# Performance work log

Measured on AMD Instinct MI355X. Metric: run time of the kernel, lower is better.

## Reference

```python
import jax, jax.numpy as jnp
import numpy as np

M, NC, NT, DX = 8, 1024, 512, 3
CHUNK = 512          # chunk_size
N_STEPS = 8          # n_steps (tol=0.0 -> torch early-stop never fires)
LR = 0.1
B1, B2, EPS = 0.9, 0.999, 1e-8
SQRT5 = 5.0 ** 0.5
LOG2PI = float(np.log(2.0 * np.pi))
NOISE_LB = 1e-4      # gpytorch GreaterThan(1e-4) noise constraint


def setup_inputs():
    key = jax.random.key(0)
    k1, k2, k3 = jax.random.split(key, 3)
    return {
        "xc": jax.random.normal(k1, (M, NC, DX), jnp.float32),
        "yc": jax.random.normal(k2, (M, NC, 1), jnp.float32),
        "xt": jax.random.normal(k3, (M, NT, DX), jnp.float32),
    }


def _kernel(x1, x2, ls, outscale):
    # ScaleKernel(MaternKernel(nu=2.5)); ls: [m,1,1], outscale: [m]
    xs1, xs2 = x1 / ls, x2 / ls
    d2 = (jnp.sum(xs1 * xs1, -1)[:, :, None]
          + jnp.sum(xs2 * xs2, -1)[:, None, :]
          - 2.0 * jnp.einsum('mnd,mkd->mnk', xs1, xs2))
    d2 = jnp.clip(d2, 1e-12, None)   # clamp like gpytorch dist for grad safety
    d = jnp.sqrt(d2)
    k = (1.0 + SQRT5 * d + (5.0 / 3.0) * d2) * jnp.exp(-SQRT5 * d)
    return outscale[:, None, None] * k


def _constrained(params):
    ls = jax.nn.softplus(params["raw_ls"])                          # [m,1,1]
    outscale = jax.nn.softplus(params["raw_os"])                    # [m]
    noise = jax.nn.softplus(params["raw_noise"][:, 0]) + NOISE_LB   # [m]
    return ls, outscale, noise


def _nll(params, x, y):
    # sum over tasks of -ExactMarginalLogLikelihood (gpytorch divides by n)
    ls, outscale, noise = _constrained(params)
    n = x.shape[1]
    K = _kernel(x, x, ls, outscale) + noise[:, None, None] * jnp.eye(n, dtype=x.dtype)
    L = jnp.linalg.cholesky(K)
    diff = y - params["const"][:, None]
    alpha = jax.scipy.linalg.cho_solve((L, True), diff[..., None])[..., 0]
    quad = jnp.sum(diff * alpha, -1)
    logdet = 2.0 * jnp.sum(jnp.log(jnp.diagonal(L, axis1=-2, axis2=-1)), -1)
    mll = -0.5 * (quad + logdet + n * LOG2PI) / n
    return jnp.sum(-mll)


def _adam_step(carry, x_sub, y_sub):
    p, m_, v_, t = carry
    g = jax.grad(_nll)(p, x_sub, y_sub)
    t = t + 1.0
    tm = jax.tree_util.tree_map
    m_ = tm(lambda a, gg: B1 * a + (1.0 - B1) * gg, m_, g)
    v_ = tm(lambda a, gg: B2 * a + (1.0 - B2) * gg * gg, v_, g)
    bc1 = 1.0 - B1 ** t
    bc2 = 1.0 - B2 ** t
    p = tm(lambda pp, mm, vv: pp - LR * (mm / bc1) / (jnp.sqrt(vv / bc2) + EPS), p, m_, v_)
    return (p, m_, v_, t)


def _gp_forward(xc, yc, xt):
    y = yc[..., 0]                                    # [m, nc]
    zl = lambda s: jnp.zeros(s, jnp.float32)
    # gpytorch raw params initialize to 0
    params = {"raw_ls": zl((M, 1, 1)), "raw_os": zl((M,)),
              "raw_noise": zl((M, 1)), "const": zl((M,))}
    m_ = jax.tree_util.tree_map(jnp.zeros_like, params)
    v_ = jax.tree_util.tree_map(jnp.zeros_like, params)
    carry = (params, m_, v_, jnp.float32(0.0))
    for i in range(0, NC, CHUNK):                     # 'Expanding' strategy
        end = min(i + CHUNK, NC)
        x_sub, y_sub = xc[:, :end], y[:, :end]
        step = lambda c, _: (_adam_step(c, x_sub, y_sub), None)
        carry, _ = jax.lax.scan(step, carry, None, length=N_STEPS)
    params = carry[0]
    # posterior predictive with trained hypers (train data = full context)
    ls, outscale, noise = _constrained(params)
    Kcc = _kernel(xc, xc, ls, outscale) + noise[:, None, None] * jnp.eye(NC, dtype=xc.dtype)
    L = jnp.linalg.cholesky(Kcc)
    diff = y - params["const"][:, None]
    alpha = jax.scipy.linalg.cho_solve((L, True), diff[..., None])[..., 0]
    Ktc = _kernel(xt, xc, ls, outscale)               # [m, nt, nc]
    mean = params["const"][:, None] + jnp.einsum('mtn,mn->mt', Ktc, alpha)
    v = jax.scipy.linalg.solve_triangular(L, jnp.swapaxes(Ktc, 1, 2), lower=True)  # [m,nc,nt]
    var_f = outscale[:, None] - jnp.sum(v * v, axis=1)  # Matern(0)=1 -> prior diag = outputscale
    var = var_f + noise[:, None]                      # likelihood(f) adds observation noise
    return jnp.stack([mean, var])                     # [2, m, nt]


def reference(xc, yc, xt):
    return _gp_forward(xc, yc, xt)
```

## Files before the change

### kernel.cpp

```cpp
#include <hip/hip_runtime.h>
#include <math.h>

constexpr int MM = 8;
constexpr int NC = 1024;
constexpr int NT = 512;
constexpr int GRID = 512;
constexpr int GPB  = GRID / MM;

constexpr size_t OFF_A     = (size_t)MM * 1024 * 1024;
constexpr size_t OFF_T     = OFF_A * 2;
constexpr size_t OFF_KTC   = OFF_T + (size_t)MM * 512 * 512;
constexpr size_t OFF_ALPHA = OFF_KTC + (size_t)MM * NT * NC;
constexpr size_t OFF_ACC   = OFF_ALPHA + (size_t)MM * 1024;

#define S5 2.2360679775f

struct GBar {
  unsigned slot[GPB][16];
  unsigned gen[16];
};
__device__ GBar g_bar2[MM];

__device__ __forceinline__ unsigned bar_base(int m) {
  return __hip_atomic_load(&g_bar2[m].gen[0], __ATOMIC_RELAXED, __HIP_MEMORY_SCOPE_AGENT);
}

__device__ __forceinline__ void gbar(int m, int gb, unsigned& ph) {
  __syncthreads();
  GBar* b = &g_bar2[m];
  const int tid = threadIdx.x;
  if (gb == 0) {
    if (tid >= 1 && tid < GPB) {
      while (__hip_atomic_load(&b->slot[tid][0], __ATOMIC_RELAXED, __HIP_MEMORY_SCOPE_AGENT) < ph)
        __builtin_amdgcn_s_sleep(2);
    }
    __syncthreads();
    if (tid == 0) {
      __threadfence();
      __hip_atomic_store(&b->gen[0], ph, __ATOMIC_RELAXED, __HIP_MEMORY_SCOPE_AGENT);
    }
    __syncthreads();
  } else {
    if (tid == 0) {
      __threadfence();
      __hip_atomic_store(&b->slot[gb][0], ph, __ATOMIC_RELAXED, __HIP_MEMORY_SCOPE_AGENT);
      while (__hip_atomic_load(&b->gen[0], __ATOMIC_RELAXED, __HIP_MEMORY_SCOPE_AGENT) < ph)
        __builtin_amdgcn_s_sleep(8);
      __threadfence();
    }
    __syncthreads();
  }
  ph++;
}

__device__ __forceinline__ float sigmf(float x) { return 1.0f / (1.0f + expf(-x)); }
__device__ __forceinline__ float softplusf(float x) { return fmaxf(x, 0.0f) + log1pf(expf(-fabsf(x))); }

__device__ __forceinline__ void lt_decode(int x, int& i, int& j) {
  int ii = 0;
  while ((ii + 1) * (ii + 2) / 2 <= x) ++ii;
  i = ii; j = x - ii * (ii + 1) / 2;
}

struct SMem {
  float Ls[64 * 65];
  float Us[64 * 65];
  float Tt[32 * 33];
  float dvec[64];
  float As[16][68];
  float Bs[16][68];
  float xi[64][3];
  float xj[64][3];
  float ai[64];
  float aj[64];
  float red[4][4];
  unsigned bar0;
};

template <int TA, int TB>
__device__ __forceinline__ void gemm64(const float* __restrict__ A, int lda,
                                       const float* __restrict__ B, int ldb,
                                       int kBeg, int kEnd, float acc[4][4], SMem& sm) {
  int tid = threadIdx.x, tx = tid & 15, ty = tid >> 4;
  float ra[4], rb[4];
  auto ldAB = [&](int k0) {
#pragma unroll
    for (int q = 0; q < 4; ++q) {
      int e = tid + (q << 8);
      if (TA) { int kk = e >> 6, r = e & 63; ra[q] = A[(size_t)(k0 + kk) * lda + r]; }
      else    { int r = e >> 4, kk = e & 15; ra[q] = A[(size_t)r * lda + k0 + kk]; }
      if (TB) { int c = e >> 4, kk = e & 15; rb[q] = B[(size_t)c * ldb + k0 + kk]; }
      else    { int kk = e >> 6, c = e & 63; rb[q] = B[(size_t)(k0 + kk) * ldb + c]; }
    }
  };
  ldAB(kBeg);
  for (int k0 = kBeg; k0 < kEnd; k0 += 16) {
    __syncthreads();
#pragma unroll
    for (int q = 0; q < 4; ++q) {
      int e = tid + (q << 8);
      if (TA) sm.As[e >> 6][e & 63] = ra[q]; else sm.As[e & 15][e >> 4] = ra[q];
      if (TB) sm.Bs[e & 15][e >> 4] = rb[q]; else sm.Bs[e >> 6][e & 63] = rb[q];
    }
    __syncthreads();
    if (k0 + 16 < kEnd) ldAB(k0 + 16);
#pragma unroll
    for (int kk = 0; kk < 16; ++kk) {
      float a[4], b[4];
#pragma unroll
      for (int i = 0; i < 4; ++i) a[i] = sm.As[kk][ty * 4 + i];
#pragma unroll
      for (int j = 0; j < 4; ++j) b[j] = sm.Bs[kk][tx * 4 + j];
#pragma unroll
      for (int i = 0; i < 4; ++i)
#pragma unroll
        for (int j = 0; j < 4; ++j) acc[i][j] = fmaf(a[i], b[j], acc[i][j]);
    }
  }
}

__device__ void factor64(SMem& sm, float* Uout, int ldu) {
  int tid = threadIdx.x;
  int tx = tid & 15, ty = tid >> 4;
  for (int j = 0; j < 63; ++j) {
    float rinv = 1.0f / sm.Ls[j * 65 + j];
    for (int i = j + 1 + ty; i < 64; i += 16) {
      float lij = sm.Ls[i * 65 + j] * rinv;
      for (int c = j + 1 + tx; c <= i; c += 16) sm.Ls[i * 65 + c] -= lij * sm.Ls[c * 65 + j];
    }
    __syncthreads();
  }
  if (tid < 64) sm.dvec[tid] = 1.0f / sqrtf(sm.Ls[tid * 65 + tid]);
  __syncthreads();
  for (int e = tid; e < 4096; e += 256) { int r = e >> 6, c = e & 63; if (c <= r) sm.Ls[r * 65 + c] *= sm.dvec[c]; }
  __syncthreads();
  for (int e = tid; e < 64 * 65; e += 256) sm.Us[e] = 0.0f;
  __syncthreads();
  if (tid < 64) {
    int b = tid >> 5, c0 = tid & 31, base = b * 32, gc = base + c0;
    sm.Us[gc * 65 + gc] = 1.0f / sm.Ls[gc * 65 + gc];
    for (int r = c0 + 1; r < 32; ++r) {
      int gr = base + r;
      float acc = 0.0f;
      for (int l = c0; l < r; ++l) acc += sm.Ls[gr * 65 + base + l] * sm.Us[(base + l) * 65 + gc];
      sm.Us[gr * 65 + gc] = -acc / sm.Ls[gr * 65 + gr];
    }
  }
  __syncthreads();
  for (int e = tid; e < 1024; e += 256) {
    int r = e >> 5, c = e & 31;
    float acc = 0.0f;
    for (int l = c; l < 32; ++l) acc += sm.Ls[(32 + r) * 65 + l] * sm.Us[l * 65 + c];
    sm.Tt[r * 33 + c] = acc;
  }
  __syncthreads();
  for (int e = tid; e < 1024; e += 256) {
    int r = e >> 5, c = e & 31;
    float acc = 0.0f;
    for (int l = 0; l <= r; ++l) acc += sm.Us[(32 + r) * 65 + 32 + l] * sm.Tt[l * 33 + c];
    sm.Us[(32 + r) * 65 + c] = -acc;
  }
  __syncthreads();
  for (int e = tid; e < 4096; e += 256) { int r = e >> 6, c = e & 63; Uout[(size_t)r * ldu + c] = sm.Us[r * 65 + c]; }
}


__device__ void adam_all(const float* __restrict__ yc, const float* __restrict__ ws,
                         int pn, int tstep, int m, int tid, SMem& sm,
                         float praw[4], float pm[4], float pv[4],
                         float& ls, float& os, float& noi, float& cm) {
  const float* al = ws + OFF_ALPHA + (size_t)m * 1024;
  const float* accp = ws + OFF_ACC + m * 8;
  const float* ym = yc + (size_t)m * NC;
  float t4 = 0, t5 = 0, t6 = 0;
  for (int i = tid; i < pn; i += 256) {
    float a = al[i];
    t4 = fmaf(a, a, t4); t5 += a; t6 = fmaf(ym[i] - cm, a, t6);
  }
  for (int off = 32; off; off >>= 1) {
    t4 += __shfl_down(t4, off); t5 += __shfl_down(t5, off); t6 += __shfl_down(t6, off);
  }
  int wid = tid >> 6, lane = tid & 63;
  if (lane == 0) { sm.red[wid][0] = t4; sm.red[wid][1] = t5; sm.red[wid][2] = t6; }
  __syncthreads();
  t4 = sm.red[0][0] + sm.red[1][0] + sm.red[2][0] + sm.red[3][0];
  t5 = sm.red[0][1] + sm.red[1][1] + sm.red[2][1] + sm.red[3][1];
  t6 = sm.red[0][2] + sm.red[1][2] + sm.red[2][2] + sm.red[3][2];
  float T1 = accp[0], T2 = accp[1], t3 = accp[2];
  float fn = (float)pn;
  float g_ls = 0.5f / fn * (T1 - T2);
  float g_os = 0.5f / (fn * os) * (fn - noi * t3 - t6 + noi * t4);
  float g_no = 0.5f / fn * (t3 - t4);
  float g_c = -t5 / fn;
  float gr[4];
  gr[0] = g_ls * sigmf(praw[0]);
  gr[1] = g_os * sigmf(praw[1]);
  gr[2] = g_no * sigmf(praw[2]);
  gr[3] = g_c;
  float bc1 = 1.0f - powf(0.9f, (float)tstep);
  float bc2 = 1.0f - powf(0.999f, (float)tstep);
#pragma unroll
  for (int i = 0; i < 4; ++i) {
    float mv = 0.9f * pm[i] + 0.1f * gr[i];
    float vv = 0.999f * pv[i] + 0.001f * gr[i] * gr[i];
    pm[i] = mv; pv[i] = vv;
    praw[i] = praw[i] - 0.1f * (mv / bc1) / (sqrtf(vv / bc2) + 1e-8f);
  }
  ls = softplusf(praw[0]);
  os = softplusf(praw[1]);
  noi = softplusf(praw[2]) + 1e-4f;
  cm = praw[3];
  __syncthreads();
}

__device__ void d_buildK(const float* __restrict__ xc, float* ws, int n, int job, int m,
                         int tid, SMem& sm, float ls, float os, float noi) {
  const float* xm = xc + (size_t)m * NC * 3;
  float* Km = ws + (size_t)m * 1048576;
  float* Am = ws + OFF_A + (size_t)m * 1048576;
  float il2 = 1.0f / (ls * ls);
  int bi, bj; lt_decode(job, bi, bj);
  if (tid < 64) {
    int r = bi * 64 + tid;
    sm.xi[tid][0] = xm[r * 3 + 0]; sm.xi[tid][1] = xm[r * 3 + 1]; sm.xi[tid][2] = xm[r * 3 + 2];
  } else if (tid < 128) {
    int lr = tid - 64; int r = bj * 64 + lr;
    sm.xj[lr][0] = xm[r * 3 + 0]; sm.xj[lr][1] = xm[r * 3 + 1]; sm.xj[lr][2] = xm[r * 3 + 2];
  }
  __syncthreads();
  if (job == 0) {
    for (int e = tid; e < 4096; e += 256) {
      int r = e >> 6, c = e & 63;
      float d0 = sm.xi[r][0] - sm.xj[c][0], d1 = sm.xi[r][1] - sm.xj[c][1], d2 = sm.xi[r][2] - sm.xj[c][2];
      float r2 = d0 * d0 + d1 * d1 + d2 * d2;
      float z = fmaxf(r2 * il2, 1e-12f);
      float dd = sqrtf(z);
      float kv = os * (1.0f + S5 * dd + (5.0f / 3.0f) * z) * expf(-S5 * dd);
      if (r == c) kv += noi;
      sm.Ls[r * 65 + c] = kv;
    }
    __syncthreads();
    factor64(sm, Am, n);
  } else {
    for (int e = tid; e < 4096; e += 256) {
      int r = e >> 6, c = e & 63;
      float d0 = sm.xi[r][0] - sm.xj[c][0], d1 = sm.xi[r][1] - sm.xj[c][1], d2 = sm.xi[r][2] - sm.xj[c][2];
      float r2 = d0 * d0 + d1 * d1 + d2 * d2;
      float z = fmaxf(r2 * il2, 1e-12f);
      float dd = sqrtf(z);
      float kv = os * (1.0f + S5 * dd + (5.0f / 3.0f) * z) * expf(-S5 * dd);
      if (bi == bj && r == c) kv += noi;
      Km[(size_t)(bi * 64 + r) * n + bj * 64 + c] = kv;
    }
  }
}

__device__ void d_trail(float* ws, int k, int n, int job, int m, int tid, SMem& sm) {
  int tx = tid & 15, ty = tid >> 4;
  float* Km = ws + (size_t)m * 1048576;
  float* Am = ws + OFF_A + (size_t)m * 1048576;
  const float* Linv = Am + (size_t)(k * 64) * n + k * 64;
  int di, dj; lt_decode(job, di, dj);
  int i = k + 1 + di, j = k + 1 + dj;
  float pp[4][4] = {};
  gemm64<0, 1>(Km + (size_t)(i * 64) * n + k * 64, n, Linv, n, 0, 64, pp, sm);
  __syncthreads();
#pragma unroll
  for (int ii = 0; ii < 4; ++ii)
#pragma unroll
    for (int jj = 0; jj < 4; ++jj) sm.Ls[(ty * 4 + ii) * 65 + tx * 4 + jj] = pp[ii][jj];
  if (di == dj) {
    float* P = Am + (size_t)(i * 64) * n + k * 64;
#pragma unroll
    for (int ii = 0; ii < 4; ++ii)
#pragma unroll
      for (int jj = 0; jj < 4; ++jj) P[(size_t)(ty * 4 + ii) * n + tx * 4 + jj] = pp[ii][jj];
  } else {
#pragma unroll
    for (int ii = 0; ii < 4; ++ii)
#pragma unroll
      for (int jj = 0; jj < 4; ++jj) pp[ii][jj] = 0.0f;
    gemm64<0, 1>(Km + (size_t)(j * 64) * n + k * 64, n, Linv, n, 0, 64, pp, sm);
#pragma unroll
    for (int ii = 0; ii < 4; ++ii)
#pragma unroll
      for (int jj = 0; jj < 4; ++jj) sm.Us[(ty * 4 + ii) * 65 + tx * 4 + jj] = pp[ii][jj];
  }
  __syncthreads();
  float acc[4][4] = {};
  {
    const float* Bsrc = (di == dj) ? sm.Ls : sm.Us;
    for (int l = 0; l < 64; ++l) {
      float a[4], b[4];
#pragma unroll
      for (int ii = 0; ii < 4; ++ii) a[ii] = sm.Ls[(ty * 4 + ii) * 65 + l];
#pragma unroll
      for (int jj = 0; jj < 4; ++jj) b[jj] = Bsrc[(tx * 4 + jj) * 65 + l];
#pragma unroll
      for (int ii = 0; ii < 4; ++ii)
#pragma unroll
        for (int jj = 0; jj < 4; ++jj) acc[ii][jj] = fmaf(a[ii], b[jj], acc[ii][jj]);
    }
  }
  float* C = Km + (size_t)(i * 64) * n + j * 64;
  if (job == 0) {
    __syncthreads();
#pragma unroll
    for (int ii = 0; ii < 4; ++ii)
#pragma unroll
      for (int jj = 0; jj < 4; ++jj)
        sm.Ls[(ty * 4 + ii) * 65 + tx * 4 + jj] =
            C[(size_t)(ty * 4 + ii) * n + tx * 4 + jj] - acc[ii][jj];
    __syncthreads();
    factor64(sm, Am + (size_t)((k + 1) * 64) * n + (k + 1) * 64, n);
  } else {
#pragma unroll
    for (int ii = 0; ii < 4; ++ii)
#pragma unroll
      for (int jj = 0; jj < 4; ++jj)
        C[(size_t)(ty * 4 + ii) * n + tx * 4 + jj] -= acc[ii][jj];
  }
}

__device__ void d_trinv64(float* ws, int n, int p, int m, int tid, SMem& sm) {
  int tx = tid & 15, ty = tid >> 4;
  float* Am = ws + OFF_A + (size_t)m * 1048576;
  int rb = (2 * p + 1) * 64, cb = 2 * p * 64;
  for (int e = tid; e < 4096; e += 256) {
    int r = e >> 6, c = e & 63;
    sm.Ls[r * 65 + c] = Am[(size_t)(rb + r) * n + cb + c];
    sm.Us[r * 65 + c] = Am[(size_t)(cb + r) * n + cb + c];
  }
  __syncthreads();
  float tt[4][4] = {};
  for (int l = 0; l < 64; ++l) {
    float a[4], b[4];
#pragma unroll
    for (int ii = 0; ii < 4; ++ii) a[ii] = sm.Ls[(ty * 4 + ii) * 65 + l];
#pragma unroll
    for (int jj = 0; jj < 4; ++jj) b[jj] = sm.Us[l * 65 + tx * 4 + jj];
#pragma unroll
    for (int ii = 0; ii < 4; ++ii)
#pragma unroll
      for (int jj = 0; jj < 4; ++jj) tt[ii][jj] = fmaf(a[ii], b[jj], tt[ii][jj]);
  }
  __syncthreads();
#pragma unroll
  for (int ii = 0; ii < 4; ++ii)
#pragma unroll
    for (int jj = 0; jj < 4; ++jj) sm.Ls[(ty * 4 + ii) * 65 + tx * 4 + jj] = tt[ii][jj];
  for (int e = tid; e < 4096; e += 256) {
    int r = e >> 6, c = e & 63;
    sm.Us[r * 65 + c] = Am[(size_t)(rb + r) * n + rb + c];
  }
  __syncthreads();
  float oo[4][4] = {};
  for (int l = 0; l < 64; ++l) {
    float a[4], b[4];
#pragma unroll
    for (int ii = 0; ii < 4; ++ii) a[ii] = sm.Us[(ty * 4 + ii) * 65 + l];
#pragma unroll
    for (int jj = 0; jj < 4; ++jj) b[jj] = sm.Ls[l * 65 + tx * 4 + jj];
#pragma unroll
    for (int ii = 0; ii < 4; ++ii)
#pragma unroll
      for (int jj = 0; jj < 4; ++jj) oo[ii][jj] = fmaf(a[ii], b[jj], oo[ii][jj]);
  }
#pragma unroll
  for (int ii = 0; ii < 4; ++ii)
#pragma unroll
    for (int jj = 0; jj < 4; ++jj)
      Am[(size_t)(rb + ty * 4 + ii) * n + cb + tx * 4 + jj] = -oo[ii][jj];
}

__device__ void d_trinvT(float* ws, int s, int n, int job, int m, int tid, SMem& sm) {
  int tx = tid & 15, ty = tid >> 4;
  float* Am = ws + OFF_A + (size_t)m * 1048576;
  float* Tm = ws + OFF_T + (size_t)m * 262144;
  int st = s >> 6;
  int p = job / (st * st), rem = job % (st * st);
  int ti = rem / st, tj = rem % st;
  int base = p * 2 * s;
  float acc[4][4] = {};
  gemm64<0, 0>(Am + (size_t)(base + s + ti * 64) * n + base, n,
               Am + (size_t)base * n + base + tj * 64, n, tj * 64, s, acc, sm);
  float* C = Tm + (size_t)p * s * s + (size_t)(ti * 64) * s + tj * 64;
#pragma unroll
  for (int ii = 0; ii < 4; ++ii)
#pragma unroll
    for (int jj = 0; jj < 4; ++jj) C[(size_t)(ty * 4 + ii) * s + tx * 4 + jj] = acc[ii][jj];
}

__device__ void d_trinvA(float* ws, int s, int n, int job, int m, int tid, SMem& sm) {
  int tx = tid & 15, ty = tid >> 4;
  float* Am = ws + OFF_A + (size_t)m * 1048576;
  const float* Tm = ws + OFF_T + (size_t)m * 262144;
  int st = s >> 6;
  int p = job / (st * st), rem = job % (st * st);
  int ti = rem / st, tj = rem % st;
  int base = p * 2 * s;
  float acc[4][4] = {};
  gemm64<0, 0>(Am + (size_t)(base + s + ti * 64) * n + base + s, n,
               Tm + (size_t)p * s * s + tj * 64, s, 0, (ti + 1) * 64, acc, sm);
  float* C = Am + (size_t)(base + s + ti * 64) * n + base + tj * 64;
#pragma unroll
  for (int ii = 0; ii < 4; ++ii)
#pragma unroll
    for (int jj = 0; jj < 4; ++jj) C[(size_t)(ty * 4 + ii) * n + tx * 4 + jj] = -acc[ii][jj];
}

__device__ void d_syrkAT(const float* __restrict__ yc, const float* __restrict__ xc,
                         float* ws, int n, int job, int m, int tid, SMem& sm,
                         float cm, float ls, float os, bool writeG) {
  int tx = tid & 15, ty = tid >> 4;
  const float* Am = ws + OFF_A + (size_t)m * 1048576;
  float* Gm = ws + (size_t)m * 1048576;
  const float* ym = yc + (size_t)m * NC;
  const float* xm = xc + (size_t)m * NC * 3;
  float* accp = ws + OFF_ACC + m * 8;
  float* al = ws + OFF_ALPHA + (size_t)m * 1024;
  int ib, jb; lt_decode(job, ib, jb);
  if (tid < 64) {
    int r = ib * 64 + tid;
    sm.ai[tid] = ym[r] - cm;
    sm.xi[tid][0] = xm[r * 3 + 0]; sm.xi[tid][1] = xm[r * 3 + 1]; sm.xi[tid][2] = xm[r * 3 + 2];
  } else if (tid < 128) {
    int lr = tid - 64; int r = jb * 64 + lr;
    sm.aj[lr] = ym[r] - cm;
    sm.xj[lr][0] = xm[r * 3 + 0]; sm.xj[lr][1] = xm[r * 3 + 1]; sm.xj[lr][2] = xm[r * 3 + 2];
  }
  float acc[4][4] = {};
  gemm64<1, 0>(Am + ib * 64, n, Am + jb * 64, n, ib * 64, n, acc, sm);
  if (writeG) {
#pragma unroll
    for (int ii = 0; ii < 4; ++ii)
#pragma unroll
      for (int jj = 0; jj < 4; ++jj) {
        int r = ty * 4 + ii, c = tx * 4 + jj;
        Gm[(size_t)(ib * 64 + r) * n + jb * 64 + c] = acc[ii][jj];
        if (ib != jb) Gm[(size_t)(jb * 64 + c) * n + ib * 64 + r] = acc[ii][jj];
      }
  }
  if (ib == jb && tx == ty) {
    atomicAdd(&accp[2], acc[0][0] + acc[1][1] + acc[2][2] + acc[3][3]);
  }
  float rowp[4];
#pragma unroll
  for (int i = 0; i < 4; ++i) {
    float s = 0.0f;
#pragma unroll
    for (int j = 0; j < 4; ++j) s = fmaf(acc[i][j], sm.aj[tx * 4 + j], s);
    rowp[i] = s;
  }
  float colp[4];
  if (ib != jb) {
#pragma unroll
    for (int j = 0; j < 4; ++j) {
      float s = 0.0f;
#pragma unroll
      for (int i = 0; i < 4; ++i) s = fmaf(acc[i][j], sm.ai[ty * 4 + i], s);
      colp[j] = s;
    }
  }
  float il2 = 1.0f / (ls * ls);
  float c53 = (5.0f / 3.0f) * os / ls;
  float a1 = 0.0f;
#pragma unroll
  for (int ii = 0; ii < 4; ++ii) {
    int r = ty * 4 + ii;
#pragma unroll
    for (int jj = 0; jj < 4; ++jj) {
      int c = tx * 4 + jj;
      float d0 = sm.xi[r][0] - sm.xj[c][0], d1 = sm.xi[r][1] - sm.xj[c][1], d2 = sm.xi[r][2] - sm.xj[c][2];
      float r2 = d0 * d0 + d1 * d1 + d2 * d2;
      float z = fmaxf(r2 * il2, 1e-12f);
      float dd = sqrtf(z);
      float Cv = c53 * z * (1.0f + S5 * dd) * expf(-S5 * dd);
      a1 = fmaf(acc[ii][jj], Cv, a1);
    }
  }
  a1 *= (ib == jb) ? 1.0f : 2.0f;
  for (int off = 32; off; off >>= 1) a1 += __shfl_down(a1, off);
  int wid = tid >> 6, lane = tid & 63;
  if (lane == 0) sm.red[wid][0] = a1;
  __syncthreads();
  if (tid == 0)
    atomicAdd(&accp[0], sm.red[0][0] + sm.red[1][0] + sm.red[2][0] + sm.red[3][0]);
  float* redA = &sm.As[0][0];
  float* redB = &sm.Bs[0][0];
#pragma unroll
  for (int i = 0; i < 4; ++i) redA[(ty * 4 + i) * 16 + tx] = rowp[i];
  if (ib != jb) {
#pragma unroll
    for (int j = 0; j < 4; ++j) redB[(tx * 4 + j) * 16 + ty] = colp[j];
  }
  __syncthreads();
  if (tid < 64) {
    float s = 0.0f;
#pragma unroll
    for (int q = 0; q < 16; ++q) s += redA[tid * 16 + q];
    atomicAdd(&al[ib * 64 + tid], s);
    if (ib != jb) {
      float s2 = 0.0f;
#pragma unroll
      for (int q = 0; q < 16; ++q) s2 += redB[tid * 16 + q];
      atomicAdd(&al[jb * 64 + tid], s2);
    }
  }
}

__device__ void d_reduce2(const float* __restrict__ xc, float* ws, int n, int job, int m,
                          int tid, SMem& sm, float ls, float os) {
  const float* xm = xc + (size_t)m * NC * 3;
  const float* al = ws + OFF_ALPHA + (size_t)m * 1024;
  float* accp = ws + OFF_ACC + m * 8;
  float il2 = 1.0f / (ls * ls);
  float c53 = (5.0f / 3.0f) * os / ls;
  int bi, bj; lt_decode(job, bi, bj);
  float w = (bi == bj) ? 1.0f : 2.0f;
  if (tid < 64) {
    int r = bi * 64 + tid;
    sm.xi[tid][0] = xm[r * 3 + 0]; sm.xi[tid][1] = xm[r * 3 + 1]; sm.xi[tid][2] = xm[r * 3 + 2];
    sm.ai[tid] = al[r];
  } else if (tid < 128) {
    int lr = tid - 64; int r = bj * 64 + lr;
    sm.xj[lr][0] = xm[r * 3 + 0]; sm.xj[lr][1] = xm[r * 3 + 1]; sm.xj[lr][2] = xm[r * 3 + 2];
    sm.aj[lr] = al[r];
  }
  __syncthreads();
  float a2 = 0.0f;
  for (int e = tid; e < 4096; e += 256) {
    int r = e >> 6, c = e & 63;
    float d0 = sm.xi[r][0] - sm.xj[c][0], d1 = sm.xi[r][1] - sm.xj[c][1], d2 = sm.xi[r][2] - sm.xj[c][2];
    float r2 = d0 * d0 + d1 * d1 + d2 * d2;
    float z = fmaxf(r2 * il2, 1e-12f);
    float dd = sqrtf(z);
    float Cv = c53 * z * (1.0f + S5 * dd) * expf(-S5 * dd);
    a2 = fmaf(sm.ai[r] * sm.aj[c], Cv, a2);
  }
  a2 *= w;
  for (int off = 32; off; off >>= 1) a2 += __shfl_down(a2, off);
  int wid = tid >> 6, lane = tid & 63;
  if (lane == 0) sm.red[wid][1] = a2;
  __syncthreads();
  if (tid == 0) {
    atomicAdd(&accp[1], sm.red[0][1] + sm.red[1][1] + sm.red[2][1] + sm.red[3][1]);
  }
}

__device__ void d_buildKtc(const float* __restrict__ xt, const float* __restrict__ xc,
                           float* ws, int job, int m, int tid, SMem& sm, float ls, float os) {
  const float* xtm = xt + (size_t)m * NT * 3;
  const float* xm = xc + (size_t)m * NC * 3;
  float* Kt = ws + OFF_KTC + (size_t)m * NT * NC;
  float* Tm = ws + OFF_T + (size_t)m * 262144;
  float il2 = 1.0f / (ls * ls);
  if (job < 2) {
    int z = job * 256 + tid;
    Tm[z] = 0.0f; Tm[NT + z] = 0.0f;
  }
  int ti = job >> 4, tj = job & 15;
  if (tid < 64) {
    int r = ti * 64 + tid;
    sm.xi[tid][0] = xtm[r * 3 + 0]; sm.xi[tid][1] = xtm[r * 3 + 1]; sm.xi[tid][2] = xtm[r * 3 + 2];
  } else if (tid < 128) {
    int lr = tid - 64; int r = tj * 64 + lr;
    sm.xj[lr][0] = xm[r * 3 + 0]; sm.xj[lr][1] = xm[r * 3 + 1]; sm.xj[lr][2] = xm[r * 3 + 2];
  }
  __syncthreads();
  for (int e = tid; e < 4096; e += 256) {
    int r = e >> 6, c = e & 63;
    float d0 = sm.xi[r][0] - sm.xj[c][0], d1 = sm.xi[r][1] - sm.xj[c][1], d2 = sm.xi[r][2] - sm.xj[c][2];
    float r2 = d0 * d0 + d1 * d1 + d2 * d2;
    float z = fmaxf(r2 * il2, 1e-12f);
    float dd = sqrtf(z);
    float kv = os * (1.0f + S5 * dd + (5.0f / 3.0f) * z) * expf(-S5 * dd);
    Kt[(size_t)(ti * 64 + r) * NC + tj * 64 + c] = kv;
  }
}

__device__ void d_predW(float* ws, int job, int m, int tid, SMem& sm) {
  int tx = tid & 15, ty = tid >> 4;
  const float* Kt = ws + OFF_KTC + (size_t)m * NT * NC;
  const float* Gm = ws + (size_t)m * 1048576;
  const float* al = ws + OFF_ALPHA + (size_t)m * 1024;
  float* S1 = ws + OFF_T + (size_t)m * 262144;
  float* S2 = S1 + NT;
  int ti = job >> 4, tj = job & 15;
  if (tid < 64) sm.aj[tid] = al[tj * 64 + tid];
  float acc[4][4] = {};
  gemm64<0, 0>(Kt + (size_t)(ti * 64) * NC, NC, Gm + tj * 64, 1024, 0, 1024, acc, sm);
  float s1p[4], s2p[4];
#pragma unroll
  for (int i = 0; i < 4; ++i) {
    float a1 = 0.0f, a2 = 0.0f;
    const float* kr = Kt + (size_t)(ti * 64 + ty * 4 + i) * NC + tj * 64;
#pragma unroll
    for (int j = 0; j < 4; ++j) {
      float kv = kr[tx * 4 + j];
      a1 = fmaf(kv, sm.aj[tx * 4 + j], a1);
      a2 = fmaf(kv, acc[i][j], a2);
    }
    s1p[i] = a1; s2p[i] = a2;
  }
  __syncthreads();
  float* redA = &sm.As[0][0];
  float* redB = &sm.Bs[0][0];
#pragma unroll
  for (int i = 0; i < 4; ++i) {
    redA[(ty * 4 + i) * 16 + tx] = s1p[i];
    redB[(ty * 4 + i) * 16 + tx] = s2p[i];
  }
  __syncthreads();
  if (tid < 64) {
    float a1 = 0.0f, a2 = 0.0f;
#pragma unroll
    for (int q = 0; q < 16; ++q) { a1 += redA[tid * 16 + q]; a2 += redB[tid * 16 + q]; }
    atomicAdd(&S1[ti * 64 + tid], a1);
    atomicAdd(&S2[ti * 64 + tid], a2);
  }
}

__global__ __launch_bounds__(256, 2) void k_gp(const float* __restrict__ xc,
                                               const float* __restrict__ yc,
                                               const float* __restrict__ xt,
                                               float* ws, float* out) {
  __shared__ SMem sm;
  const int bid = blockIdx.x;
  const int m  = bid % MM;
  const int gb = bid / MM;
  const int tid = threadIdx.x;

  if (tid == 0) sm.bar0 = bar_base(m);
  __syncthreads();
  unsigned ph = sm.bar0 + 1;

  float praw[4] = {0.f, 0.f, 0.f, 0.f};
  float pm[4]   = {0.f, 0.f, 0.f, 0.f};
  float pv[4]   = {0.f, 0.f, 0.f, 0.f};
  float ls = 0.69314718056f, os = 0.69314718056f;
  float noi = 0.69314718056f + 1e-4f, cm = 0.0f;

  for (int step = 0; step < 17; ++step) {
    const int n = step < 8 ? 512 : 1024;
    const int nb = n >> 6;
    const bool lastStep = (step == 16);

    if (step > 0) {
      adam_all(yc, ws, step <= 8 ? 512 : 1024, step, m, tid, sm,
               praw, pm, pv, ls, os, noi, cm);
    }
    {
      const int tot = nb * (nb + 1) / 2;
      if (gb == 0) {
        __syncthreads();
        d_buildK(xc, ws, n, 0, m, tid, sm, ls, os, noi);
      } else {
        for (int q = gb; q < tot; q += GPB - 1) {
          __syncthreads();
          d_buildK(xc, ws, n, q, m, tid, sm, ls, os, noi);
        }
      }
      gbar(m, gb, ph);
    }

    for (int k = 0; k <= nb - 2; ++k) {
      const int t = nb - 1 - k;
      const int tot = t * (t + 1) / 2;
      if (gb == 0) {
        if (k == 0) {
          float* al = ws + OFF_ALPHA + (size_t)m * 1024;
          for (int z = tid; z < 1024; z += 256) al[z] = 0.0f;
          if (tid < 8) ws[OFF_ACC + m * 8 + tid] = 0.0f;
        }
        __syncthreads();
        d_trail(ws, k, n, 0, m, tid, sm);
      } else {
        for (int q = gb; q < tot; q += GPB - 1) {
          __syncthreads();
          d_trail(ws, k, n, q, m, tid, sm);
        }
        if ((k & 1) && gb == GPB - 1) {
          __syncthreads();
          d_trinv64(ws, n, k >> 1, m, tid, sm);
        }
      }
      gbar(m, gb, ph);
    }

    for (int s = 128; s < n; s <<= 1) {
      const int st = s >> 6;
      const int np = n / (2 * s);
      const int tot = np * st * st;
      for (int q = gb; q < tot; q += GPB) {
        __syncthreads();
        d_trinvT(ws, s, n, q, m, tid, sm);
      }
      if (s == 128 && gb == GPB - 1) {
        __syncthreads();
        d_trinv64(ws, n, nb / 2 - 1, m, tid, sm);
      }
      gbar(m, gb, ph);
      for (int q = gb; q < tot; q += GPB) {
        __syncthreads();
        d_trinvA(ws, s, n, q, m, tid, sm);
      }
      gbar(m, gb, ph);
    }

    {
      const int tot = nb * (nb + 1) / 2;
      for (int q = gb; q < tot; q += GPB) {
        __syncthreads();
        d_syrkAT(yc, xc, ws, n, q, m, tid, sm, cm, ls, os, lastStep);
      }
      gbar(m, gb, ph);
    }

    if (step < 16) {
      const int tot = nb * (nb + 1) / 2;
      for (int q = gb; q < tot; q += GPB) {
        __syncthreads();
        d_reduce2(xc, ws, n, q, m, tid, sm, ls, os);
      }
      gbar(m, gb, ph);
    }
  }

  {
    for (int q = gb; q < 128; q += GPB) {
      __syncthreads();
      d_buildKtc(xt, xc, ws, q, m, tid, sm, ls, os);
    }
    gbar(m, gb, ph);
    for (int q = gb; q < 128; q += GPB) {
      __syncthreads();
      d_predW(ws, q, m, tid, sm);
    }
    gbar(m, gb, ph);
    const float* S1 = ws + OFF_T + (size_t)m * 262144;
    const float* S2 = S1 + NT;
    for (int t = gb * 256 + tid; t < NT; t += GPB * 256) {
      out[(size_t)m * NT + t] = cm + S1[t];
      out[(size_t)MM * NT + (size_t)m * NT + t] = os + noi - S2[t];
    }
  }
}

extern "C" void kernel_launch(void* const* d_in, const int* in_sizes, int n_in,
                              void* d_out, int out_size, void* d_ws, size_t ws_size,
                              hipStream_t stream) {
  const float* xc = (const float*)d_in[0];
  const float* yc = (const float*)d_in[1];
  const float* xt = (const float*)d_in[2];
  float* out = (float*)d_out;
  float* ws = (float*)d_ws;

  hipLaunchKernelGGL(k_gp, dim3(GRID), dim3(256), 0, stream, xc, yc, xt, ws, out);

  (void)in_sizes; (void)n_in; (void)out_size; (void)ws_size;
}
```

Before: 22.36 ms.

## Use fence-free grid barrier when all blocks of a task share one XCD

At startup each block records its XCC ID from a hardware register. After a full barrier, every task group checks whether all of its blocks landed on the same XCD. If so, later barriers drop the __threadfence and only wait for outstanding memory ops (s_waitcnt vmcnt(0)) before signalling. Reads of workspace data written by other blocks become volatile so they skip stale L1 lines. This aims to cut the cost of the many grid barriers per Adam step, but volatile loads may stop vectorisation and caching in the GEMM and other tile loads. Whether the cheap path runs at all depends on how blocks are placed across XCDs.

```diff
diff --git a/kernel.cpp b/kernel.cpp
--- a/kernel.cpp
+++ b/kernel.cpp
@@ -18,6 +18,7 @@
 struct GBar {
   unsigned slot[GPB][16];
   unsigned gen[16];
+  unsigned xcd[GPB][16];
 };
 __device__ GBar g_bar2[MM];
 
@@ -25,7 +26,7 @@
   return __hip_atomic_load(&g_bar2[m].gen[0], __ATOMIC_RELAXED, __HIP_MEMORY_SCOPE_AGENT);
 }
 
-__device__ __forceinline__ void gbar(int m, int gb, unsigned& ph) {
+__device__ __forceinline__ void gbar_full(int m, int gb, unsigned ph) {
   __syncthreads();
   GBar* b = &g_bar2[m];
   const int tid = threadIdx.x;
@@ -50,6 +51,36 @@
     }
     __syncthreads();
   }
+}
+
+__device__ __forceinline__ void gbar_cheap(int m, int gb, unsigned ph) {
+  __syncthreads();
+  GBar* b = &g_bar2[m];
+  const int tid = threadIdx.x;
+  if (gb == 0) {
+    if (tid >= 1 && tid < GPB) {
+      while (__hip_atomic_load(&b->slot[tid][0], __ATOMIC_RELAXED, __HIP_MEMORY_SCOPE_AGENT) < ph)
+        __builtin_amdgcn_s_sleep(2);
+    }
+    __syncthreads();
+    if (tid == 0) {
+      asm volatile("s_waitcnt vmcnt(0)" ::: "memory");
+      __hip_atomic_store(&b->gen[0], ph, __ATOMIC_RELAXED, __HIP_MEMORY_SCOPE_AGENT);
+    }
+    __syncthreads();
+  } else {
+    if (tid == 0) {
+      asm volatile("s_waitcnt vmcnt(0)" ::: "memory");
+      __hip_atomic_store(&b->slot[gb][0], ph, __ATOMIC_RELAXED, __HIP_MEMORY_SCOPE_AGENT);
+      while (__hip_atomic_load(&b->gen[0], __ATOMIC_RELAXED, __HIP_MEMORY_SCOPE_AGENT) < ph)
+        __builtin_amdgcn_s_sleep(8);
+    }
+    __syncthreads();
+  }
+}
+
+__device__ __forceinline__ void gbar(int m, int gb, unsigned& ph, int cheap) {
+  if (cheap) gbar_cheap(m, gb, ph); else gbar_full(m, gb, ph);
   ph++;
 }
 
@@ -75,11 +106,12 @@
   float aj[64];
   float red[4][4];
   unsigned bar0;
+  int cheap;
 };
 
 template <int TA, int TB>
-__device__ __forceinline__ void gemm64(const float* __restrict__ A, int lda,
-                                       const float* __restrict__ B, int ldb,
+__device__ __forceinline__ void gemm64(const volatile float* __restrict__ A, int lda,
+                                       const volatile float* __restrict__ B, int ldb,
                                        int kBeg, int kEnd, float acc[4][4], SMem& sm) {
   int tid = threadIdx.x, tx = tid & 15, ty = tid >> 4;
   float ra[4], rb[4];
@@ -169,8 +201,8 @@
                          int pn, int tstep, int m, int tid, SMem& sm,
                          float praw[4], float pm[4], float pv[4],
                          float& ls, float& os, float& noi, float& cm) {
-  const float* al = ws + OFF_ALPHA + (size_t)m * 1024;
-  const float* accp = ws + OFF_ACC + m * 8;
+  const volatile float* al = ws + OFF_ALPHA + (size_t)m * 1024;
+  const volatile float* accp = ws + OFF_ACC + m * 8;
   const float* ym = yc + (size_t)m * NC;
   float t4 = 0, t5 = 0, t6 = 0;
   for (int i = tid; i < pn; i += 256) {
@@ -259,7 +291,7 @@
   int tx = tid & 15, ty = tid >> 4;
   float* Km = ws + (size_t)m * 1048576;
   float* Am = ws + OFF_A + (size_t)m * 1048576;
-  const float* Linv = Am + (size_t)(k * 64) * n + k * 64;
+  const volatile float* Linv = Am + (size_t)(k * 64) * n + k * 64;
   int di, dj; lt_decode(job, di, dj);
   int i = k + 1 + di, j = k + 1 + dj;
   float pp[4][4] = {};
@@ -304,32 +336,36 @@
   }
   float* C = Km + (size_t)(i * 64) * n + j * 64;
   if (job == 0) {
+    const volatile float* Cv = C;
     __syncthreads();
 #pragma unroll
     for (int ii = 0; ii < 4; ++ii)
 #pragma unroll
       for (int jj = 0; jj < 4; ++jj)
         sm.Ls[(ty * 4 + ii) * 65 + tx * 4 + jj] =
-            C[(size_t)(ty * 4 + ii) * n + tx * 4 + jj] - acc[ii][jj];
+            Cv[(size_t)(ty * 4 + ii) * n + tx * 4 + jj] - acc[ii][jj];
     __syncthreads();
     factor64(sm, Am + (size_t)((k + 1) * 64) * n + (k + 1) * 64, n);
   } else {
+    const volatile float* Cv = C;
 #pragma unroll
     for (int ii = 0; ii < 4; ++ii)
 #pragma unroll
       for (int jj = 0; jj < 4; ++jj)
-        C[(size_t)(ty * 4 + ii) * n + tx * 4 + jj] -= acc[ii][jj];
+        C[(size_t)(ty * 4 + ii) * n + tx * 4 + jj] =
+            Cv[(size_t)(ty * 4 + ii) * n + tx * 4 + jj] - acc[ii][jj];
   }
 }
 
 __device__ void d_trinv64(float* ws, int n, int p, int m, int tid, SMem& sm) {
   int tx = tid & 15, ty = tid >> 4;
   float* Am = ws + OFF_A + (size_t)m * 1048576;
+  const volatile float* Av = Am;
   int rb = (2 * p + 1) * 64, cb = 2 * p * 64;
   for (int e = tid; e < 4096; e += 256) {
     int r = e >> 6, c = e & 63;
-    sm.Ls[r * 65 + c] = Am[(size_t)(rb + r) * n + cb + c];
-    sm.Us[r * 65 + c] = Am[(size_t)(cb + r) * n + cb + c];
+    sm.Ls[r * 65 + c] = Av[(size_t)(rb + r) * n + cb + c];
+    sm.Us[r * 65 + c] = Av[(size_t)(cb + r) * n + cb + c];
   }
   __syncthreads();
   float tt[4][4] = {};
@@ -351,7 +387,7 @@
     for (int jj = 0; jj < 4; ++jj) sm.Ls[(ty * 4 + ii) * 65 + tx * 4 + jj] = tt[ii][jj];
   for (int e = tid; e < 4096; e += 256) {
     int r = e >> 6, c = e & 63;
-    sm.Us[r * 65 + c] = Am[(size_t)(rb + r) * n + rb + c];
+    sm.Us[r * 65 + c] = Av[(size_t)(rb + r) * n + rb + c];
   }
   __syncthreads();
   float oo[4][4] = {};
@@ -394,7 +430,7 @@
 __device__ void d_trinvA(float* ws, int s, int n, int job, int m, int tid, SMem& sm) {
   int tx = tid & 15, ty = tid >> 4;
   float* Am = ws + OFF_A + (size_t)m * 1048576;
-  const float* Tm = ws + OFF_T + (size_t)m * 262144;
+  const volatile float* Tm = ws + OFF_T + (size_t)m * 262144;
   int st = s >> 6;
   int p = job / (st * st), rem = job % (st * st);
   int ti = rem / st, tj = rem % st;
@@ -512,7 +548,7 @@
 __device__ void d_reduce2(const float* __restrict__ xc, float* ws, int n, int job, int m,
                           int tid, SMem& sm, float ls, float os) {
   const float* xm = xc + (size_t)m * NC * 3;
-  const float* al = ws + OFF_ALPHA + (size_t)m * 1024;
+  const volatile float* al = ws + OFF_ALPHA + (size_t)m * 1024;
   float* accp = ws + OFF_ACC + m * 8;
   float il2 = 1.0f / (ls * ls);
   float c53 = (5.0f / 3.0f) * os / ls;
@@ -581,9 +617,9 @@
 
 __device__ void d_predW(float* ws, int job, int m, int tid, SMem& sm) {
   int tx = tid & 15, ty = tid >> 4;
-  const float* Kt = ws + OFF_KTC + (size_t)m * NT * NC;
-  const float* Gm = ws + (size_t)m * 1048576;
-  const float* al = ws + OFF_ALPHA + (size_t)m * 1024;
+  const volatile float* Kt = ws + OFF_KTC + (size_t)m * NT * NC;
+  const volatile float* Gm = ws + (size_t)m * 1048576;
+  const volatile float* al = ws + OFF_ALPHA + (size_t)m * 1024;
   float* S1 = ws + OFF_T + (size_t)m * 262144;
   float* S2 = S1 + NT;
   int ti = job >> 4, tj = job & 15;
@@ -594,7 +630,7 @@
 #pragma unroll
   for (int i = 0; i < 4; ++i) {
     float a1 = 0.0f, a2 = 0.0f;
-    const float* kr = Kt + (size_t)(ti * 64 + ty * 4 + i) * NC + tj * 64;
+    const volatile float* kr = Kt + (size_t)(ti * 64 + ty * 4 + i) * NC + tj * 64;
 #pragma unroll
     for (int j = 0; j < 4; ++j) {
       float kv = kr[tx * 4 + j];
@@ -634,6 +670,22 @@
   if (tid == 0) sm.bar0 = bar_base(m);
   __syncthreads();
   unsigned ph = sm.bar0 + 1;
+
+  if (tid == 0) {
+    unsigned x;
+    asm volatile("s_getreg_b32 %0, hwreg(HW_REG_XCC_ID)" : "=s"(x));
+    __hip_atomic_store(&g_bar2[m].xcd[gb][0], x, __ATOMIC_RELAXED, __HIP_MEMORY_SCOPE_AGENT);
+  }
+  gbar_full(m, gb, ph);
+  ph++;
+  if (tid < GPB) {
+    unsigned v = __hip_atomic_load(&g_bar2[m].xcd[tid][0], __ATOMIC_RELAXED, __HIP_MEMORY_SCOPE_AGENT);
+    unsigned v0 = __shfl(v, 0, 64);
+    unsigned long long bal = __ballot(v == v0);
+    if (tid == 0) sm.cheap = (bal == ~0ull) ? 1 : 0;
+  }
+  __syncthreads();
+  const int cheap = sm.cheap;
 
   float praw[4] = {0.f, 0.f, 0.f, 0.f};
   float pm[4]   = {0.f, 0.f, 0.f, 0.f};
@@ -661,7 +713,7 @@
           d_buildK(xc, ws, n, q, m, tid, sm, ls, os, noi);
         }
       }
-      gbar(m, gb, ph);
+      gbar(m, gb, ph, cheap);
     }
 
     for (int k = 0; k <= nb - 2; ++k) {
@@ -685,7 +737,7 @@
           d_trinv64(ws, n, k >> 1, m, tid, sm);
         }
       }
-      gbar(m, gb, ph);
+      gbar(m, gb, ph, cheap);
     }
 
     for (int s = 128; s < n; s <<= 1) {
@@ -700,12 +752,12 @@
         __syncthreads();
         d_trinv64(ws, n, nb / 2 - 1, m, tid, sm);
       }
-      gbar(m, gb, ph);
+      gbar(m, gb, ph, cheap);
       for (int q = gb; q < tot; q += GPB) {
         __syncthreads();
         d_trinvA(ws, s, n, q, m, tid, sm);
       }
-      gbar(m, gb, ph);
+      gbar(m, gb, ph, cheap);
     }
 
     {
@@ -714,7 +766,7 @@
         __syncthreads();
         d_syrkAT(yc, xc, ws, n, q, m, tid, sm, cm, ls, os, lastStep);
       }
-      gbar(m, gb, ph);
+      gbar(m, gb, ph, cheap);
     }
 
     if (step < 16) {
@@ -723,7 +775,7 @@
         __syncthreads();
         d_reduce2(xc, ws, n, q, m, tid, sm, ls, os);
       }
-      gbar(m, gb, ph);
+      gbar(m, gb, ph, cheap);
     }
   }
 
@@ -732,14 +784,14 @@
       __syncthreads();
       d_buildKtc(xt, xc, ws, q, m, tid, sm, ls, os);
     }
-    gbar(m, gb, ph);
+    gbar(m, gb, ph, cheap);
     for (int q = gb; q < 128; q += GPB) {
       __syncthreads();
       d_predW(ws, q, m, tid, sm);
     }
-    gbar(m, gb, ph);
-    const float* S1 = ws + OFF_T + (size_t)m * 262144;
-    const float* S2 = S1 + NT;
+    gbar(m, gb, ph, cheap);
+    const volatile float* S1 = ws + OFF_T + (size_t)m * 262144;
+    const volatile float* S2 = S1 + NT;
     for (int t = gb * 256 + tid; t < NT; t += GPB * 256) {
       out[(size_t)m * NT + t] = cm + S1[t];
       out[(size_t)MM * NT + (size_t)m * NT + t] = os + noi - S2[t];
```

Result: faster. 21.46 ms (-4.0%).
